# Optimization experiments

Measured on AMD Instinct MI355X. Metric: run time of the kernel, lower is better.

Reference implementation:

```python
import jax, jax.numpy as jnp
import numpy as np
from jax import lax

BS, CNT, W, P, E, K, L = 32, 128, 2048, 1024, 8, 25, 2


def setup_inputs() -> dict:
    key = jax.random.key(0)
    ks = jax.random.split(key, 12)
    s = lambda k, shape, scale: jax.random.normal(k, shape, dtype=jnp.float32) * scale
    return {
        "x": s(ks[0], (BS, CNT, W), 1.0),
        "conv_w": s(ks[1], (L, E, 1, K), 0.2),
        "conv_b": s(ks[2], (L, E), 0.02),
        "wq": s(ks[3], (L, P, W), 0.02),
        "bq": s(ks[4], (L, P), 0.02),
        "wk": s(ks[5], (L, P, W), 0.02),
        "bk": s(ks[6], (L, P), 0.02),
        "wv": s(ks[7], (L, P, W), 0.02),
        "bv": s(ks[8], (L, P), 0.02),
        "wo": s(ks[9], (L, W, P), 0.02),
        "bo": s(ks[10], (L, W), 0.02),
    }


def _moe(x, w, b):
    # x: [bs, cnt, W]; w: [E, 1, K]; b: [E]
    bs, cnt, d = x.shape
    xf = x.reshape(bs * cnt, 1, d)
    pad = K // 2
    y = lax.conv_general_dilated(
        xf, w, window_strides=(1,), padding=[(pad, pad)],
        dimension_numbers=("NCH", "OIH", "NCH"))  # [bs*cnt, E, W]
    y = y + b[None, :, None]
    return y.mean(axis=1).reshape(bs, cnt, d)


def _fe(x, wq, bq, wk, bk, wv, bv, wo, bo):
    # x: [bs, cnt, W]; projections to P, FFT-domain attention, back to W
    q = jnp.einsum("bcw,pw->bcp", x, wq) + bq
    k = jnp.einsum("bcw,pw->bcp", x, wk) + bk
    v = jnp.einsum("bcw,pw->bcp", x, wv) + bv
    q_fft = jnp.fft.fft(q, axis=-1)
    k_fft = jnp.fft.fft(k, axis=-1)
    v_fft = jnp.fft.fft(v, axis=-1)
    scale = jnp.sqrt(jnp.float32(P))
    weighted = (k_fft * jnp.conj(q_fft)) / scale * v_fft
    wv_real = jnp.fft.ifft(weighted, axis=-1).real.astype(x.dtype)
    return jnp.einsum("bcp,wp->bcw", wv_real, wo) + bo


def reference(x, conv_w, conv_b, wq, bq, wk, bk, wv, bv, wo, bo):
    for l in range(L):
        x = _moe(x, conv_w[l], conv_b[l])
        x = _fe(x, wq[l], bq[l], wk[l], bk[l], wv[l], bv[l], wo[l], bo[l])
    return x
```

## Files before the change

### kernel.cpp

```cpp
#include <hip/hip_runtime.h>
#include <hip/hip_bf16.h>

#define BSZ 32
#define CNTS 128
#define WD 2048
#define PD 1024
#define ED 8
#define KSZ 25
#define LN 2
#define MROWS (BSZ*CNTS)
#define QKVN (3*PD)

typedef _Float16 f16;
typedef __attribute__((ext_vector_type(8))) _Float16 f16x8;
typedef __attribute__((ext_vector_type(4))) float f32x4;
typedef __attribute__((ext_vector_type(2))) float f32x2;

#define PI_F 3.14159265358979323846f
#define PAD(a) ((a) + ((a) >> 5))

__global__ __launch_bounds__(256) void cvt_f16(
    const float* __restrict__ src, f16* __restrict__ dst, int n)
{
    const int i = (blockIdx.x * 256 + threadIdx.x) * 4;
    if (i >= n) return;
    const float4 v = *(const float4*)(src + i);
    f16 o[4];
    o[0] = (f16)v.x; o[1] = (f16)v.y; o[2] = (f16)v.z; o[3] = (f16)v.w;
    *(ushort4*)(dst + i) = *(const ushort4*)o;
}

__global__ __launch_bounds__(256) void conv_moe(
    const float* __restrict__ xin,
    const float* __restrict__ cw,
    const float* __restrict__ cb,
    f16* __restrict__ xo)
{
    __shared__ float srow[WD];
    __shared__ float swb[KSZ];
    __shared__ float sbb;
    const int tid = threadIdx.x;
    const size_t row = blockIdx.x;
    if (tid < KSZ) {
        float s = 0.f;
        for (int e = 0; e < ED; ++e) s += cw[e*KSZ + tid];
        swb[tid] = s * (1.f/ED);
    }
    if (tid == 32) {
        float s = 0.f;
        for (int e = 0; e < ED; ++e) s += cb[e];
        sbb = s * (1.f/ED);
    }
    const float* xr = xin + row*WD;
    for (int i = tid; i < WD; i += 256) srow[i] = xr[i];
    __syncthreads();
    const float bb = sbb;
    for (int t0 = 0; t0 < WD; t0 += 256) {
        const int t = t0 + tid;
        float acc = bb;
        #pragma unroll
        for (int k = 0; k < KSZ; ++k) {
            const int idx = t + k - (KSZ/2);
            const float xv = (idx >= 0 && idx < WD) ? srow[idx] : 0.f;
            acc = fmaf(xv, swb[k], acc);
        }
        xo[row*WD + t] = (f16)acc;
    }
}

__global__ __launch_bounds__(256, 2) void gemm_f16(
    const f16* __restrict__ A,
    const f16* __restrict__ B,
    const float* __restrict__ c0, const float* __restrict__ c1, const float* __restrict__ c2,
    float* __restrict__ out,
    const int K, const int N)
{
    __shared__ f16 sA[128*32];
    __shared__ f16 sB[128*32];
    const int tid  = threadIdx.x;
    const int m0   = blockIdx.x * 128;
    const int n0   = blockIdx.y * 128;
    const int lane = tid & 63;
    const int wave = tid >> 6;
    const int wm   = (wave >> 1) * 64;
    const int wn   = (wave & 1) * 64;
    const int quad = lane >> 4;
    const int r16  = lane & 15;

    f32x4 acc[4][4] = {};

    const int ci0 = tid, ci1 = 256 + tid;
    const int ra0 = ci0 >> 2, ca0 = (ci0 & 3) * 8;
    const int ra1 = ci1 >> 2, ca1 = (ci1 & 3) * 8;

    for (int kb = 0; kb < K; kb += 32) {
        const f16* gA0 = A + (size_t)(m0 + ra0) * K + kb + ca0;
        const f16* gA1 = A + (size_t)(m0 + ra1) * K + kb + ca1;
        const f16* gB0 = B + (size_t)(n0 + ra0) * K + kb + ca0;
        const f16* gB1 = B + (size_t)(n0 + ra1) * K + kb + ca1;
        __builtin_amdgcn_global_load_lds((const __attribute__((address_space(1))) unsigned int*)gA0,
            (__attribute__((address_space(3))) unsigned int*)&sA[ci0*8], 16, 0, 0);
        __builtin_amdgcn_global_load_lds((const __attribute__((address_space(1))) unsigned int*)gA1,
            (__attribute__((address_space(3))) unsigned int*)&sA[ci1*8], 16, 0, 0);
        __builtin_amdgcn_global_load_lds((const __attribute__((address_space(1))) unsigned int*)gB0,
            (__attribute__((address_space(3))) unsigned int*)&sB[ci0*8], 16, 0, 0);
        __builtin_amdgcn_global_load_lds((const __attribute__((address_space(1))) unsigned int*)gB1,
            (__attribute__((address_space(3))) unsigned int*)&sB[ci1*8], 16, 0, 0);
        __syncthreads();

        f16x8 af[4], bfm[4];
        #pragma unroll
        for (int i = 0; i < 4; ++i)
            af[i] = *(const f16x8*)&sA[(wm + i*16 + r16)*32 + quad*8];
        #pragma unroll
        for (int j = 0; j < 4; ++j)
            bfm[j] = *(const f16x8*)&sB[(wn + j*16 + r16)*32 + quad*8];
        #pragma unroll
        for (int i = 0; i < 4; ++i)
            #pragma unroll
            for (int j = 0; j < 4; ++j)
                acc[i][j] = __builtin_amdgcn_mfma_f32_16x16x32_f16(af[i], bfm[j], acc[i][j], 0, 0, 0);
        __syncthreads();
    }

    #pragma unroll
    for (int j = 0; j < 4; ++j) {
        const int col = n0 + wn + j*16 + r16;
        const float bv = (col < 1024) ? c0[col] : (col < 2048) ? c1[col-1024] : c2[col-2048];
        #pragma unroll
        for (int i = 0; i < 4; ++i) {
            #pragma unroll
            for (int r = 0; r < 4; ++r) {
                const int rowg = m0 + wm + i*16 + quad*4 + r;
                out[(size_t)rowg*N + col] = acc[i][j][r] + bv;
            }
        }
    }
}

__device__ inline void fft1024r4(f32x2* x, f32x2* y, const int tid)
{
    f32x2* src = x;
    f32x2* dst = y;
    #pragma unroll
    for (int st = 0; st < 5; ++st) {
        const int ls = 2*st;
        const int s  = 1 << ls;
        const int p  = tid >> ls;
        const int q  = tid & (s - 1);
        const float invn = 1.f / (float)(1024 >> ls);
        const f32x2 a = src[PAD(tid)];
        const f32x2 b = src[PAD(tid + 256)];
        const f32x2 c = src[PAD(tid + 512)];
        const f32x2 d = src[PAD(tid + 768)];
        float ws, wc;
        __sincosf(-2.f*PI_F * (float)p * invn, &ws, &wc);
        const float apcx = a.x + c.x, apcy = a.y + c.y;
        const float amcx = a.x - c.x, amcy = a.y - c.y;
        const float bpdx = b.x + d.x, bpdy = b.y + d.y;
        const float bmdx = b.x - d.x, bmdy = b.y - d.y;
        f32x2 y0; y0.x = apcx + bpdx; y0.y = apcy + bpdy;
        const float t1x = amcx + bmdy, t1y = amcy - bmdx;
        const float t2x = apcx - bpdx, t2y = apcy - bpdy;
        const float t3x = amcx - bmdy, t3y = amcy + bmdx;
        const float w2x = wc*wc - ws*ws, w2y = 2.f*wc*ws;
        const float w3x = w2x*wc - w2y*ws, w3y = w2x*ws + w2y*wc;
        f32x2 y1; y1.x = wc*t1x - ws*t1y;   y1.y = wc*t1y + ws*t1x;
        f32x2 y2; y2.x = w2x*t2x - w2y*t2y; y2.y = w2x*t2y + w2y*t2x;
        f32x2 y3; y3.x = w3x*t3x - w3y*t3y; y3.y = w3x*t3y + w3y*t3x;
        const int base = q + ((p * s) << 2);
        dst[PAD(base)]       = y0;
        dst[PAD(base + s)]   = y1;
        dst[PAD(base + 2*s)] = y2;
        dst[PAD(base + 3*s)] = y3;
        __syncthreads();
        f32x2* t = src; src = dst; dst = t;
    }
}

__global__ __launch_bounds__(256) void fft_attn2(
    const float* __restrict__ qkv, f16* __restrict__ outg)
{
    __shared__ f32x2 X[PAD(1023)+1], Y[PAD(1023)+1];
    const int tid = threadIdx.x;
    const size_t row0 = (size_t)blockIdx.x * 2;
    const float* r1 = qkv + row0*QKVN;
    const float* r2 = r1 + QKVN;

    f32x2 V1[4], V2[4], S1[4], S2[4];

    #pragma unroll
    for (int k = 0; k < 4; ++k) {
        const int i = tid + 256*k;
        f32x2 t; t.x = r1[2048+i]; t.y = r2[2048+i];
        X[PAD(i)] = t;
    }
    __syncthreads();
    fft1024r4(X, Y, tid);
    #pragma unroll
    for (int k = 0; k < 4; ++k) {
        const int f = tid + 256*k;
        const int g = (PD - f) & (PD-1);
        const f32x2 z1 = Y[PAD(f)], z2 = Y[PAD(g)];
        V1[k].x = 0.5f*(z1.x + z2.x); V1[k].y = 0.5f*(z1.y - z2.y);
        V2[k].x = 0.5f*(z1.y + z2.y); V2[k].y = 0.5f*(z2.x - z1.x);
    }

    #pragma unroll
    for (int k = 0; k < 4; ++k) {
        const int i = tid + 256*k;
        f32x2 t; t.x = r1[i]; t.y = r1[1024+i];
        X[PAD(i)] = t;
    }
    __syncthreads();
    fft1024r4(X, Y, tid);
    #pragma unroll
    for (int k = 0; k < 4; ++k) {
        const int f = tid + 256*k;
        const int g = (PD - f) & (PD-1);
        const f32x2 z1 = Y[PAD(f)], z2 = Y[PAD(g)];
        const float Qr = 0.5f*(z1.x + z2.x), Qi = 0.5f*(z1.y - z2.y);
        const float Kr = 0.5f*(z1.y + z2.y), Ki = 0.5f*(z2.x - z1.x);
        const float Pr = (Kr*Qr + Ki*Qi) * (1.f/32.f);
        const float Pi = (Ki*Qr - Kr*Qi) * (1.f/32.f);
        S1[k].x = Pr*V1[k].x - Pi*V1[k].y;
        S1[k].y = -(Pr*V1[k].y + Pi*V1[k].x);
    }

    #pragma unroll
    for (int k = 0; k < 4; ++k) {
        const int i = tid + 256*k;
        f32x2 t; t.x = r2[i]; t.y = r2[1024+i];
        X[PAD(i)] = t;
    }
    __syncthreads();
    fft1024r4(X, Y, tid);
    #pragma unroll
    for (int k = 0; k < 4; ++k) {
        const int f = tid + 256*k;
        const int g = (PD - f) & (PD-1);
        const f32x2 z1 = Y[PAD(f)], z2 = Y[PAD(g)];
        const float Qr = 0.5f*(z1.x + z2.x), Qi = 0.5f*(z1.y - z2.y);
        const float Kr = 0.5f*(z1.y + z2.y), Ki = 0.5f*(z2.x - z1.x);
        const float Pr = (Kr*Qr + Ki*Qi) * (1.f/32.f);
        const float Pi = (Ki*Qr - Kr*Qi) * (1.f/32.f);
        S2[k].x = Pr*V2[k].x - Pi*V2[k].y;
        S2[k].y = -(Pr*V2[k].y + Pi*V2[k].x);
    }

    #pragma unroll
    for (int k = 0; k < 4; ++k) {
        const int f = tid + 256*k;
        f32x2 t; t.x = S1[k].x - S2[k].y; t.y = S1[k].y + S2[k].x;
        X[PAD(f)] = t;
    }
    __syncthreads();
    fft1024r4(X, Y, tid);
    f16* o1 = outg + row0*PD;
    f16* o2 = o1 + PD;
    #pragma unroll
    for (int k = 0; k < 4; ++k) {
        const int n = tid + 256*k;
        const f32x2 z = Y[PAD(n)];
        o1[n] = (f16)(z.x * (1.f/1024.f));
        o2[n] = (f16)(z.y * (1.f/1024.f));
    }
}

extern "C" void kernel_launch(void* const* d_in, const int* in_sizes, int n_in,
                              void* d_out, int out_size, void* d_ws, size_t ws_size,
                              hipStream_t stream)
{
    const float* x      = (const float*)d_in[0];
    const float* conv_w = (const float*)d_in[1];
    const float* conv_b = (const float*)d_in[2];
    const float* wq     = (const float*)d_in[3];
    const float* bq     = (const float*)d_in[4];
    const float* wk     = (const float*)d_in[5];
    const float* bk     = (const float*)d_in[6];
    const float* wv     = (const float*)d_in[7];
    const float* bv     = (const float*)d_in[8];
    const float* wo     = (const float*)d_in[9];
    const float* bo     = (const float*)d_in[10];

    char* ws = (char*)d_ws;
    const size_t MB = 1024*1024;
    f16*   wqkv16 = (f16*)(ws);
    f16*   wo16   = (f16*)(ws + 12*MB);
    float* qkvbuf = (float*)(ws + 16*MB);
    float* xmid   = (float*)(ws + 64*MB);
    f16*   xc16   = (f16*)(ws + 96*MB);
    f16*   wvr16  = xc16;

    const int NWL = PD * WD;
    const dim3 cvtg(NWL/4/256);

    for (int l = 0; l < LN; ++l) {
        cvt_f16<<<cvtg, dim3(256), 0, stream>>>(wq + (size_t)l*NWL, wqkv16,                   NWL);
        cvt_f16<<<cvtg, dim3(256), 0, stream>>>(wk + (size_t)l*NWL, wqkv16 + (size_t)PD*WD,   NWL);
        cvt_f16<<<cvtg, dim3(256), 0, stream>>>(wv + (size_t)l*NWL, wqkv16 + (size_t)2*PD*WD, NWL);
        cvt_f16<<<cvtg, dim3(256), 0, stream>>>(wo + (size_t)l*NWL, wo16, NWL);

        const float* xin = (l == 0) ? x : xmid;
        conv_moe<<<dim3(MROWS), dim3(256), 0, stream>>>(
            xin, conv_w + (size_t)l*ED*KSZ, conv_b + (size_t)l*ED, xc16);

        gemm_f16<<<dim3(MROWS/128, QKVN/128), dim3(256), 0, stream>>>(
            xc16, wqkv16,
            bq + (size_t)l*PD, bk + (size_t)l*PD, bv + (size_t)l*PD,
            qkvbuf, WD, QKVN);

        fft_attn2<<<dim3(MROWS/2), dim3(256), 0, stream>>>(qkvbuf, wvr16);

        float* xout = (l == LN-1) ? (float*)d_out : xmid;
        gemm_f16<<<dim3(MROWS/128, WD/128), dim3(256), 0, stream>>>(
            wvr16, wo16,
            bo + (size_t)l*WD, bo + (size_t)l*WD + PD, bo + (size_t)l*WD + PD,
            xout, PD, WD);
    }
}
```

Measured before the change: 439.1 us.

## Use f16 intermediates, widen GEMM K-tile with XOR swizzle, fuse weight conversions

The qkv buffer and the inter-layer activation are now stored in f16 instead of f32, which halves the traffic written by the GEMMs and read by the FFT and conv kernels. The GEMM K-tile grows from 32 to 64 and the LDS layout gets an XOR swizzle, so there are half as many barriers and fewer bank conflicts. The four per-layer weight conversion launches become one. The cost is reduced precision in the intermediates, and the larger LDS footprint may lower occupancy.

```diff
diff --git a/kernel.cpp b/kernel.cpp
--- a/kernel.cpp
+++ b/kernel.cpp
@@ -10,6 +10,7 @@
 #define LN 2
 #define MROWS (BSZ*CNTS)
 #define QKVN (3*PD)
+#define NWL (PD*WD)
 
 typedef _Float16 f16;
 typedef __attribute__((ext_vector_type(8))) _Float16 f16x8;
@@ -19,19 +20,30 @@
 #define PI_F 3.14159265358979323846f
 #define PAD(a) ((a) + ((a) >> 5))
 
-__global__ __launch_bounds__(256) void cvt_f16(
-    const float* __restrict__ src, f16* __restrict__ dst, int n)
+__global__ __launch_bounds__(256) void cvt_layer(
+    const float* __restrict__ wq, const float* __restrict__ wk,
+    const float* __restrict__ wv, const float* __restrict__ wo,
+    f16* __restrict__ wqkv16, f16* __restrict__ wo16)
 {
     const int i = (blockIdx.x * 256 + threadIdx.x) * 4;
-    if (i >= n) return;
-    const float4 v = *(const float4*)(src + i);
+    const float* src;
+    f16* dst;
+    if (i < 3*NWL) {
+        dst = wqkv16 + i;
+        src = (i < NWL) ? wq + i : (i < 2*NWL) ? wk + (i - NWL) : wv + (i - 2*NWL);
+    } else {
+        dst = wo16 + (i - 3*NWL);
+        src = wo + (i - 3*NWL);
+    }
+    const float4 v = *(const float4*)src;
     f16 o[4];
     o[0] = (f16)v.x; o[1] = (f16)v.y; o[2] = (f16)v.z; o[3] = (f16)v.w;
-    *(ushort4*)(dst + i) = *(const ushort4*)o;
-}
-
+    *(ushort4*)dst = *(const ushort4*)o;
+}
+
+template<typename IT>
 __global__ __launch_bounds__(256) void conv_moe(
-    const float* __restrict__ xin,
+    const IT* __restrict__ xin,
     const float* __restrict__ cw,
     const float* __restrict__ cb,
     f16* __restrict__ xo)
@@ -51,8 +63,8 @@
         for (int e = 0; e < ED; ++e) s += cb[e];
         sbb = s * (1.f/ED);
     }
-    const float* xr = xin + row*WD;
-    for (int i = tid; i < WD; i += 256) srow[i] = xr[i];
+    const IT* xr = xin + row*WD;
+    for (int i = tid; i < WD; i += 256) srow[i] = (float)xr[i];
     __syncthreads();
     const float bb = sbb;
     for (int t0 = 0; t0 < WD; t0 += 256) {
@@ -68,15 +80,16 @@
     }
 }
 
+template<typename OT>
 __global__ __launch_bounds__(256, 2) void gemm_f16(
     const f16* __restrict__ A,
     const f16* __restrict__ B,
     const float* __restrict__ c0, const float* __restrict__ c1, const float* __restrict__ c2,
-    float* __restrict__ out,
+    OT* __restrict__ out,
     const int K, const int N)
 {
-    __shared__ f16 sA[128*32];
-    __shared__ f16 sB[128*32];
+    __shared__ f16 sA[128*64];
+    __shared__ f16 sB[128*64];
     const int tid  = threadIdx.x;
     const int m0   = blockIdx.x * 128;
     const int n0   = blockIdx.y * 128;
@@ -89,37 +102,57 @@
 
     f32x4 acc[4][4] = {};
 
-    const int ci0 = tid, ci1 = 256 + tid;
-    const int ra0 = ci0 >> 2, ca0 = (ci0 & 3) * 8;
-    const int ra1 = ci1 >> 2, ca1 = (ci1 & 3) * 8;
-
-    for (int kb = 0; kb < K; kb += 32) {
-        const f16* gA0 = A + (size_t)(m0 + ra0) * K + kb + ca0;
-        const f16* gA1 = A + (size_t)(m0 + ra1) * K + kb + ca1;
-        const f16* gB0 = B + (size_t)(n0 + ra0) * K + kb + ca0;
-        const f16* gB1 = B + (size_t)(n0 + ra1) * K + kb + ca1;
-        __builtin_amdgcn_global_load_lds((const __attribute__((address_space(1))) unsigned int*)gA0,
-            (__attribute__((address_space(3))) unsigned int*)&sA[ci0*8], 16, 0, 0);
-        __builtin_amdgcn_global_load_lds((const __attribute__((address_space(1))) unsigned int*)gA1,
-            (__attribute__((address_space(3))) unsigned int*)&sA[ci1*8], 16, 0, 0);
-        __builtin_amdgcn_global_load_lds((const __attribute__((address_space(1))) unsigned int*)gB0,
-            (__attribute__((address_space(3))) unsigned int*)&sB[ci0*8], 16, 0, 0);
-        __builtin_amdgcn_global_load_lds((const __attribute__((address_space(1))) unsigned int*)gB1,
-            (__attribute__((address_space(3))) unsigned int*)&sB[ci1*8], 16, 0, 0);
+    int arow[4], aoff[4];
+    #pragma unroll
+    for (int t = 0; t < 4; ++t) {
+        const int s = tid + 256*t;
+        const int row = s >> 3;
+        const int sc8 = ((s & 7) ^ (row & 7)) * 8;
+        arow[t] = row;
+        aoff[t] = row * K + sc8;
+    }
+
+    int aBase[4], aXor[4], bBase[4], bXor[4];
+    #pragma unroll
+    for (int i = 0; i < 4; ++i) {
+        const int ra = wm + i*16 + r16;
+        aBase[i] = ra << 3; aXor[i] = ra & 7;
+        const int rb = wn + i*16 + r16;
+        bBase[i] = rb << 3; bXor[i] = rb & 7;
+    }
+
+    const size_t mK = (size_t)m0 * K;
+    const size_t nK = (size_t)n0 * K;
+
+    for (int kb = 0; kb < K; kb += 64) {
+        #pragma unroll
+        for (int t = 0; t < 4; ++t) {
+            const int s = tid + 256*t;
+            __builtin_amdgcn_global_load_lds(
+                (const __attribute__((address_space(1))) unsigned int*)(A + mK + aoff[t] + kb),
+                (__attribute__((address_space(3))) unsigned int*)&sA[s*8], 16, 0, 0);
+            __builtin_amdgcn_global_load_lds(
+                (const __attribute__((address_space(1))) unsigned int*)(B + nK + aoff[t] + kb),
+                (__attribute__((address_space(3))) unsigned int*)&sB[s*8], 16, 0, 0);
+        }
         __syncthreads();
 
-        f16x8 af[4], bfm[4];
         #pragma unroll
-        for (int i = 0; i < 4; ++i)
-            af[i] = *(const f16x8*)&sA[(wm + i*16 + r16)*32 + quad*8];
-        #pragma unroll
-        for (int j = 0; j < 4; ++j)
-            bfm[j] = *(const f16x8*)&sB[(wn + j*16 + r16)*32 + quad*8];
-        #pragma unroll
-        for (int i = 0; i < 4; ++i)
+        for (int ks = 0; ks < 2; ++ks) {
+            const int c = ks*4 + quad;
+            f16x8 af[4], bfm[4];
+            #pragma unroll
+            for (int i = 0; i < 4; ++i)
+                af[i] = *(const f16x8*)&sA[(aBase[i] | (c ^ aXor[i])) * 8];
             #pragma unroll
             for (int j = 0; j < 4; ++j)
-                acc[i][j] = __builtin_amdgcn_mfma_f32_16x16x32_f16(af[i], bfm[j], acc[i][j], 0, 0, 0);
+                bfm[j] = *(const f16x8*)&sB[(bBase[j] | (c ^ bXor[j])) * 8];
+            #pragma unroll
+            for (int i = 0; i < 4; ++i)
+                #pragma unroll
+                for (int j = 0; j < 4; ++j)
+                    acc[i][j] = __builtin_amdgcn_mfma_f32_16x16x32_f16(af[i], bfm[j], acc[i][j], 0, 0, 0);
+        }
         __syncthreads();
     }
 
@@ -132,7 +165,7 @@
             #pragma unroll
             for (int r = 0; r < 4; ++r) {
                 const int rowg = m0 + wm + i*16 + quad*4 + r;
-                out[(size_t)rowg*N + col] = acc[i][j][r] + bv;
+                out[(size_t)rowg*N + col] = (OT)(acc[i][j][r] + bv);
             }
         }
     }
@@ -179,20 +212,20 @@
 }
 
 __global__ __launch_bounds__(256) void fft_attn2(
-    const float* __restrict__ qkv, f16* __restrict__ outg)
+    const f16* __restrict__ qkv, f16* __restrict__ outg)
 {
     __shared__ f32x2 X[PAD(1023)+1], Y[PAD(1023)+1];
     const int tid = threadIdx.x;
     const size_t row0 = (size_t)blockIdx.x * 2;
-    const float* r1 = qkv + row0*QKVN;
-    const float* r2 = r1 + QKVN;
+    const f16* r1 = qkv + row0*QKVN;
+    const f16* r2 = r1 + QKVN;
 
     f32x2 V1[4], V2[4], S1[4], S2[4];
 
     #pragma unroll
     for (int k = 0; k < 4; ++k) {
         const int i = tid + 256*k;
-        f32x2 t; t.x = r1[2048+i]; t.y = r2[2048+i];
+        f32x2 t; t.x = (float)r1[2048+i]; t.y = (float)r2[2048+i];
         X[PAD(i)] = t;
     }
     __syncthreads();
@@ -209,7 +242,7 @@
     #pragma unroll
     for (int k = 0; k < 4; ++k) {
         const int i = tid + 256*k;
-        f32x2 t; t.x = r1[i]; t.y = r1[1024+i];
+        f32x2 t; t.x = (float)r1[i]; t.y = (float)r1[1024+i];
         X[PAD(i)] = t;
     }
     __syncthreads();
@@ -230,7 +263,7 @@
     #pragma unroll
     for (int k = 0; k < 4; ++k) {
         const int i = tid + 256*k;
-        f32x2 t; t.x = r2[i]; t.y = r2[1024+i];
+        f32x2 t; t.x = (float)r2[i]; t.y = (float)r2[1024+i];
         X[PAD(i)] = t;
     }
     __syncthreads();
@@ -287,35 +320,39 @@
     const size_t MB = 1024*1024;
     f16*   wqkv16 = (f16*)(ws);
     f16*   wo16   = (f16*)(ws + 12*MB);
-    float* qkvbuf = (float*)(ws + 16*MB);
-    float* xmid   = (float*)(ws + 64*MB);
-    f16*   xc16   = (f16*)(ws + 96*MB);
+    f16*   qkvbuf = (f16*)(ws + 16*MB);
+    f16*   xc16   = (f16*)(ws + 40*MB);
+    f16*   xmid   = (f16*)(ws + 56*MB);
     f16*   wvr16  = xc16;
 
-    const int NWL = PD * WD;
-    const dim3 cvtg(NWL/4/256);
-
     for (int l = 0; l < LN; ++l) {
-        cvt_f16<<<cvtg, dim3(256), 0, stream>>>(wq + (size_t)l*NWL, wqkv16,                   NWL);
-        cvt_f16<<<cvtg, dim3(256), 0, stream>>>(wk + (size_t)l*NWL, wqkv16 + (size_t)PD*WD,   NWL);
-        cvt_f16<<<cvtg, dim3(256), 0, stream>>>(wv + (size_t)l*NWL, wqkv16 + (size_t)2*PD*WD, NWL);
-        cvt_f16<<<cvtg, dim3(256), 0, stream>>>(wo + (size_t)l*NWL, wo16, NWL);
-
-        const float* xin = (l == 0) ? x : xmid;
-        conv_moe<<<dim3(MROWS), dim3(256), 0, stream>>>(
-            xin, conv_w + (size_t)l*ED*KSZ, conv_b + (size_t)l*ED, xc16);
-
-        gemm_f16<<<dim3(MROWS/128, QKVN/128), dim3(256), 0, stream>>>(
+        cvt_layer<<<dim3(4*NWL/4/256), dim3(256), 0, stream>>>(
+            wq + (size_t)l*NWL, wk + (size_t)l*NWL, wv + (size_t)l*NWL, wo + (size_t)l*NWL,
+            wqkv16, wo16);
+
+        if (l == 0)
+            conv_moe<float><<<dim3(MROWS), dim3(256), 0, stream>>>(
+                x, conv_w, conv_b, xc16);
+        else
+            conv_moe<f16><<<dim3(MROWS), dim3(256), 0, stream>>>(
+                xmid, conv_w + (size_t)l*ED*KSZ, conv_b + (size_t)l*ED, xc16);
+
+        gemm_f16<f16><<<dim3(MROWS/128, QKVN/128), dim3(256), 0, stream>>>(
             xc16, wqkv16,
             bq + (size_t)l*PD, bk + (size_t)l*PD, bv + (size_t)l*PD,
             qkvbuf, WD, QKVN);
 
         fft_attn2<<<dim3(MROWS/2), dim3(256), 0, stream>>>(qkvbuf, wvr16);
 
-        float* xout = (l == LN-1) ? (float*)d_out : xmid;
-        gemm_f16<<<dim3(MROWS/128, WD/128), dim3(256), 0, stream>>>(
-            wvr16, wo16,
-            bo + (size_t)l*WD, bo + (size_t)l*WD + PD, bo + (size_t)l*WD + PD,
-            xout, PD, WD);
-    }
-}
+        if (l == LN-1)
+            gemm_f16<float><<<dim3(MROWS/128, WD/128), dim3(256), 0, stream>>>(
+                wvr16, wo16,
+                bo + (size_t)l*WD, bo + (size_t)l*WD + PD, bo + (size_t)l*WD + PD,
+                (float*)d_out, PD, WD);
+        else
+            gemm_f16<f16><<<dim3(MROWS/128, WD/128), dim3(256), 0, stream>>>(
+                wvr16, wo16,
+                bo + (size_t)l*WD, bo + (size_t)l*WD + PD, bo + (size_t)l*WD + PD,
+                xmid, PD, WD);
+    }
+}
```

After: 413.9 us. 5.7% less time.
